# Optimization experiments

Measured on AMD Instinct MI355X. Metric: run time of the kernel, lower is better.

The kernel has to match this reference:

```python
import jax, jax.numpy as jnp
import numpy as np

TOP_K = 2

def setup_inputs() -> dict:
    key = jax.random.key(0)
    ks = jax.random.split(key, 8)
    B, S, D = 2, 2048, 1024
    N_r, N_s = 16, 2
    u = jax.random.normal(ks[0], (B, S, D), dtype=jnp.float32)
    centroids = jax.random.normal(ks[1], (N_r, D), dtype=jnp.float32)
    expert_biases = jnp.zeros((N_r,), dtype=jnp.float32)
    # routed expert Linear params: y = u @ W.T + b, W stored [E, d_out, d_in]
    Wr = jax.random.normal(ks[2], (N_r, D, D), dtype=jnp.float32) * (1.0 / np.sqrt(D))
    br = jax.random.normal(ks[3], (N_r, D), dtype=jnp.float32) * 0.01
    Ws = jax.random.normal(ks[4], (N_s, D, D), dtype=jnp.float32) * (1.0 / np.sqrt(D))
    bs = jax.random.normal(ks[5], (N_s, D), dtype=jnp.float32) * 0.01
    return {"u": u, "centroids": centroids, "expert_biases": expert_biases,
            "Wr": Wr, "br": br, "Ws": Ws, "bs": bs}

def reference(u, centroids, expert_biases, Wr, br, Ws, bs):
    N_r = centroids.shape[0]
    N_s = Ws.shape[0]
    # routing scores over experts
    raw_scores = jnp.einsum('bsd,ed->bse', u, centroids)          # [B,S,E]
    s = jax.nn.softmax(raw_scores + expert_biases, axis=-1)
    # scatter top-k softmax values (un-renormalized, as in the source) into gates
    topk_vals, topk_idx = jax.lax.top_k(s, TOP_K)                  # [B,S,K]
    g_topk = jnp.sum(jax.nn.one_hot(topk_idx, N_r, dtype=s.dtype) * topk_vals[..., None], axis=-2)  # [B,S,E]
    # dense per-expert Linear for all tokens, then gated combine (faithful to source)
    xe = jnp.einsum('bsd,eod->bseo', u, Wr) + br                   # [B,S,E,D]
    routed = jnp.einsum('bse,bseo->bso', g_topk, xe)               # [B,S,D]
    # shared experts: mean of N_s dense Linears
    shared = (jnp.einsum('bsd,eod->bso', u, Ws) + jnp.sum(bs, axis=0)) / N_s
    return u + routed + shared
```

## Files before the change

kernel.cpp:

```cpp
#include <hip/hip_runtime.h>

typedef unsigned short u16x8 __attribute__((ext_vector_type(8)));
typedef short          s16x8 __attribute__((ext_vector_type(8)));
typedef float          f32x4 __attribute__((ext_vector_type(4)));

#define NTOK   4096
#define DMODEL 1024
#define NEXP   16
#define TOPK   2
#define BK     32
#define NK     (DMODEL / BK)
#define MAXT   128

__device__ inline unsigned short f2bf(float f) {
    unsigned int x = __float_as_uint(f);
    x += 0x7fffu + ((x >> 16) & 1u);
    return (unsigned short)(x >> 16);
}
__device__ inline float bf2f(unsigned short h) {
    unsigned int x = ((unsigned int)h) << 16;
    return __uint_as_float(x);
}

__device__ inline void gld16(const void* g, void* l) {
    __builtin_amdgcn_global_load_lds(
        (const __attribute__((address_space(1))) void*)g,
        (__attribute__((address_space(3))) void*)l, 16, 0, 0);
}

#define NWR8  (NEXP * DMODEL * DMODEL / 8)
#define NWS8  (DMODEL * DMODEL / 8)
#define NB8   ((NEXP + 1) * DMODEL / 8)
#define RBLK  (NTOK / 4)
#define CBLK  ((NWR8 + NWS8 + NB8 + 255) / 256)

__global__ void prep_kernel(const float* __restrict__ u,
                            const float* __restrict__ cent,
                            const float* __restrict__ ebias,
                            const float* __restrict__ Wr,
                            const float* __restrict__ br,
                            const float* __restrict__ Ws,
                            const float* __restrict__ bs,
                            unsigned short* __restrict__ ub,
                            unsigned short* __restrict__ w17,
                            float* __restrict__ b17,
                            float* __restrict__ topk_g,
                            int*   __restrict__ topk_i) {
    int bid = blockIdx.x;
    if (bid >= RBLK) {
        int id = (bid - RBLK) * 256 + threadIdx.x;
        if (id < NWR8) {
            size_t base = (size_t)id * 8;
            f32x4 a = *(const f32x4*)&Wr[base];
            f32x4 b = *(const f32x4*)&Wr[base + 4];
            u16x8 o;
#pragma unroll
            for (int i = 0; i < 4; i++) { o[i] = f2bf(a[i]); o[i + 4] = f2bf(b[i]); }
            *(u16x8*)&w17[base] = o;
        } else if (id < NWR8 + NWS8) {
            size_t base = (size_t)(id - NWR8) * 8;
            f32x4 a0 = *(const f32x4*)&Ws[base];
            f32x4 b0 = *(const f32x4*)&Ws[base + 4];
            f32x4 a1 = *(const f32x4*)&Ws[(size_t)DMODEL * DMODEL + base];
            f32x4 b1 = *(const f32x4*)&Ws[(size_t)DMODEL * DMODEL + base + 4];
            u16x8 o;
#pragma unroll
            for (int i = 0; i < 4; i++) {
                o[i]     = f2bf(a0[i] + a1[i]);
                o[i + 4] = f2bf(b0[i] + b1[i]);
            }
            *(u16x8*)&w17[(size_t)NEXP * DMODEL * DMODEL + base] = o;
        } else if (id < NWR8 + NWS8 + NB8) {
            int base = (id - NWR8 - NWS8) * 8;
#pragma unroll
            for (int i = 0; i < 8; i++) {
                int idx = base + i;
                b17[idx] = idx < NEXP * DMODEL
                    ? br[idx]
                    : bs[idx - NEXP * DMODEL] + bs[idx - NEXP * DMODEL + DMODEL];
            }
        }
        return;
    }
    int wid  = threadIdx.x >> 6;
    int lane = threadIdx.x & 63;
    int t = bid * 4 + wid;
    const float* urow = u + (size_t)t * DMODEL;

    double acc[NEXP];
#pragma unroll
    for (int e = 0; e < NEXP; e++) acc[e] = 0.0;

    for (int j = 0; j < DMODEL / 64; j++) {
        int d = j * 64 + lane;
        float uf = urow[d];
        ub[(size_t)t * DMODEL + d] = f2bf(uf);
        double uv = (double)uf;
#pragma unroll
        for (int e = 0; e < NEXP; e++)
            acc[e] += uv * (double)cent[e * DMODEL + d];
    }
#pragma unroll
    for (int e = 0; e < NEXP; e++) {
        for (int off = 32; off; off >>= 1)
            acc[e] += __shfl_xor(acc[e], off);
    }
    if (lane == 0) {
        double mx = -1e300;
#pragma unroll
        for (int e = 0; e < NEXP; e++) {
            acc[e] += (double)ebias[e];
            if (acc[e] > mx) mx = acc[e];
        }
        double ex[NEXP], den = 0.0;
#pragma unroll
        for (int e = 0; e < NEXP; e++) { ex[e] = exp(acc[e] - mx); den += ex[e]; }
        int i1 = -1, i2 = -1;
        double v1 = -1.0, v2 = -1.0;
        for (int e = 0; e < NEXP; e++) {
            double v = ex[e];
            if (v > v1)      { v2 = v1; i2 = i1; v1 = v; i1 = e; }
            else if (v > v2) { v2 = v;  i2 = e; }
        }
        topk_g[t * 2 + 0] = (float)(v1 / den);
        topk_g[t * 2 + 1] = (float)(v2 / den);
        topk_i[t * 2 + 0] = i1;
        topk_i[t * 2 + 1] = i2;
    }
}

__global__ void build_all(const float* __restrict__ topk_g,
                          const int*   __restrict__ topk_i,
                          int* __restrict__ cnt,
                          int* __restrict__ tokL,
                          float* __restrict__ gateL,
                          int* __restrict__ idL,
                          int* __restrict__ desc,
                          int* __restrict__ numT) {
    __shared__ int scnt[NEXP];
    int tid = threadIdx.x;
    if (tid < NEXP) scnt[tid] = 0;
    __syncthreads();
    for (int id = tid; id < NTOK * TOPK; id += 1024) {
        int e = topk_i[id];
        int pos = atomicAdd(&scnt[e], 1);
        tokL[e * NTOK + pos]  = id >> 1;
        gateL[e * NTOK + pos] = topk_g[id];
        idL[e * NTOK + pos]   = id;
    }
    __syncthreads();
    if (tid == 0) {
        int s = 0;
        for (int mt = 0; mt < NTOK / 128; mt++) desc[s++] = (NEXP << 16) | mt;
        for (int e = 0; e < NEXP; e++) {
            cnt[e] = scnt[e];
            int nt = (scnt[e] + 127) >> 7;
            for (int m = 0; m < nt; m++) desc[s++] = (e << 16) | m;
        }
        numT[0] = s;
    }
}

__global__ __launch_bounds__(256, 4)
void moe_gemm(const unsigned short* __restrict__ ub,
              const unsigned short* __restrict__ w17,
              const float* __restrict__ b17,
              const int*   __restrict__ cnt,
              const int*   __restrict__ tokL,
              const float* __restrict__ gateL,
              const int*   __restrict__ idL,
              const int*   __restrict__ desc,
              const int*   __restrict__ numT,
              const float* __restrict__ u,
              float* __restrict__ out,
              unsigned short* __restrict__ y) {
    int bid = blockIdx.x;
    int tile = bid >> 3;
    int n0 = (bid & 7) * 128;
    if (tile >= numT[0]) return;
    int d = desc[tile];
    int e = d >> 16;
    int row0 = (d & 0xffff) << 7;
    bool is_shared = (e == NEXP);
    int count = is_shared ? NTOK : cnt[e];

    __shared__ __align__(16) unsigned short As[2][128 * BK];
    __shared__ __align__(16) unsigned short Bs[2][128 * BK];

    int t = threadIdx.x;
    int lane = t & 63, wid = t >> 6;
    int wm = wid >> 1, wn = wid & 1;
    int lr = lane & 15, lk4 = lane >> 4;
    int rchunk = (lk4 ^ ((lr >> 1) & 3)) * 8;

    int srow = lane >> 2;
    int scs  = ((lane & 3) ^ ((lane >> 3) & 3)) * 8;

    const int* tl = tokL + e * NTOK;
    const unsigned short* asrc[2];
    const unsigned short* bsrc[2];
    const unsigned short* bb = w17 + (size_t)e * DMODEL * DMODEL + (size_t)n0 * DMODEL;
#pragma unroll
    for (int p = 0; p < 2; p++) {
        int gi = row0 + wid * 32 + p * 16 + srow;
        int tok = is_shared ? gi : tl[gi < count ? gi : count - 1];
        asrc[p] = ub + (size_t)tok * DMODEL + scs;
        bsrc[p] = bb + (size_t)(wid * 32 + p * 16 + srow) * DMODEL + scs;
    }

#define STAGE(buf, kt) do {                                                     \
    int _k0 = (kt) * BK;                                                        \
    _Pragma("unroll")                                                           \
    for (int p = 0; p < 2; p++) {                                               \
        int r = wid * 32 + p * 16;                                              \
        gld16(asrc[p] + _k0, &As[buf][r * BK]);                                 \
        gld16(bsrc[p] + _k0, &Bs[buf][r * BK]);                                 \
    } } while (0)

    f32x4 acc[4][4];
#pragma unroll
    for (int i = 0; i < 4; i++)
#pragma unroll
        for (int j = 0; j < 4; j++)
#pragma unroll
            for (int v = 0; v < 4; v++) acc[i][j][v] = 0.0f;

    STAGE(0, 0);
    int cur = 0;
    for (int kt = 0; kt < NK; kt++) {
        if (kt + 1 < NK) {
            STAGE(cur ^ 1, kt + 1);
            asm volatile("s_waitcnt vmcnt(4)" ::: "memory");
        } else {
            asm volatile("s_waitcnt vmcnt(0)" ::: "memory");
        }
        __builtin_amdgcn_s_barrier();

        __builtin_amdgcn_s_setprio(1);
        s16x8 b[4];
#pragma unroll
        for (int j = 0; j < 4; j++)
            b[j] = *(const s16x8*)&Bs[cur][(wn * 64 + j * 16 + lr) * BK + rchunk];
#pragma unroll
        for (int i = 0; i < 4; i++) {
            s16x8 a = *(const s16x8*)&As[cur][(wm * 64 + i * 16 + lr) * BK + rchunk];
#pragma unroll
            for (int j = 0; j < 4; j++)
                acc[i][j] = __builtin_amdgcn_mfma_f32_16x16x32_bf16(a, b[j], acc[i][j], 0, 0, 0);
        }
        __builtin_amdgcn_s_setprio(0);

        asm volatile("" ::: "memory");
        __builtin_amdgcn_s_barrier();
        cur ^= 1;
    }
#undef STAGE

    const float* be = b17 + e * DMODEL;
    if (is_shared) {
#pragma unroll
        for (int i = 0; i < 4; i++) {
#pragma unroll
            for (int v = 0; v < 4; v++) {
                int row = row0 + wm * 64 + i * 16 + lk4 * 4 + v;
#pragma unroll
                for (int j = 0; j < 4; j++) {
                    int col = n0 + wn * 64 + j * 16 + lr;
                    size_t idx = (size_t)row * DMODEL + col;
                    out[idx] = u[idx] + 0.5f * (acc[i][j][v] + be[col]);
                }
            }
        }
    } else {
#pragma unroll
        for (int i = 0; i < 4; i++) {
#pragma unroll
            for (int v = 0; v < 4; v++) {
                int gi = row0 + wm * 64 + i * 16 + lk4 * 4 + v;
                if (gi < count) {
                    int id = idL[e * NTOK + gi];
                    float g = gateL[e * NTOK + gi];
                    unsigned short* yr = y + (size_t)id * DMODEL;
#pragma unroll
                    for (int j = 0; j < 4; j++) {
                        int col = n0 + wn * 64 + j * 16 + lr;
                        yr[col] = f2bf(g * (acc[i][j][v] + be[col]));
                    }
                }
            }
        }
    }
}

__global__ void combine_kernel(const unsigned short* __restrict__ y,
                               float* __restrict__ out) {
    int idx = blockIdx.x * 256 + threadIdx.x;
    int tk = idx >> 7;
    int d8 = (idx & 127) * 8;
    size_t base = (size_t)tk * DMODEL + d8;
    u16x8 a = *(const u16x8*)&y[(size_t)(tk * 2) * DMODEL + d8];
    u16x8 b = *(const u16x8*)&y[(size_t)(tk * 2 + 1) * DMODEL + d8];
    f32x4 o0 = *(const f32x4*)&out[base];
    f32x4 o1 = *(const f32x4*)&out[base + 4];
#pragma unroll
    for (int v = 0; v < 4; v++) {
        o0[v] += bf2f(a[v]) + bf2f(b[v]);
        o1[v] += bf2f(a[v + 4]) + bf2f(b[v + 4]);
    }
    *(f32x4*)&out[base] = o0;
    *(f32x4*)&out[base + 4] = o1;
}

extern "C" void kernel_launch(void* const* d_in, const int* in_sizes, int n_in,
                              void* d_out, int out_size, void* d_ws, size_t ws_size,
                              hipStream_t stream) {
    const float* u    = (const float*)d_in[0];
    const float* cent = (const float*)d_in[1];
    const float* eb   = (const float*)d_in[2];
    const float* Wr   = (const float*)d_in[3];
    const float* br   = (const float*)d_in[4];
    const float* Ws   = (const float*)d_in[5];
    const float* bs   = (const float*)d_in[6];
    float* out = (float*)d_out;

    char* ws = (char*)d_ws;
    size_t off = 0;
    auto take = [&](size_t b) { size_t o = off; off += (b + 255) & ~(size_t)255; return o; };
    float* topk_g = (float*)(ws + take(NTOK * TOPK * 4));
    int*   topk_i = (int*)  (ws + take(NTOK * TOPK * 4));
    int*   cnt    = (int*)  (ws + take(64 * 4));
    int*   tokL   = (int*)  (ws + take((size_t)NEXP * NTOK * 4));
    float* gateL  = (float*)(ws + take((size_t)NEXP * NTOK * 4));
    int*   idL    = (int*)  (ws + take((size_t)NEXP * NTOK * 4));
    int*   desc   = (int*)  (ws + take(MAXT * 4));
    int*   numT   = (int*)  (ws + take(64));
    float* b17    = (float*)(ws + take((size_t)(NEXP + 1) * DMODEL * 4));
    unsigned short* ub  = (unsigned short*)(ws + take((size_t)NTOK * DMODEL * 2));
    unsigned short* w17 = (unsigned short*)(ws + take((size_t)(NEXP + 1) * DMODEL * DMODEL * 2));
    unsigned short* y   = (unsigned short*)(ws + take((size_t)NTOK * TOPK * DMODEL * 2));

    prep_kernel<<<RBLK + CBLK, 256, 0, stream>>>(
        u, cent, eb, Wr, br, Ws, bs, ub, w17, b17, topk_g, topk_i);
    build_all<<<1, 1024, 0, stream>>>(topk_g, topk_i, cnt, tokL, gateL, idL, desc, numT);
    moe_gemm<<<8 * MAXT, 256, 0, stream>>>(
        ub, w17, b17, cnt, tokL, gateL, idL, desc, numT, u, out, y);
    combine_kernel<<<(NTOK * DMODEL / 8) / 256, 256, 0, stream>>>(y, out);
}
```

Before: 100.0 us.

## Enlarge MoE GEMM tiles to 256x256x64 and parallelize expert bucketing

```diff
diff --git a/kernel.cpp b/kernel.cpp
--- a/kernel.cpp
+++ b/kernel.cpp
@@ -8,9 +8,9 @@
 #define DMODEL 1024
 #define NEXP   16
 #define TOPK   2
-#define BK     32
-#define NK     (DMODEL / BK)
-#define MAXT   128
+#define BKG    64
+#define NKT    (DMODEL / BKG)
+#define MAXT2  64
 
 __device__ inline unsigned short f2bf(float f) {
     unsigned int x = __float_as_uint(f);
@@ -129,39 +129,37 @@
     }
 }
 
-__global__ void build_all(const float* __restrict__ topk_g,
-                          const int*   __restrict__ topk_i,
-                          int* __restrict__ cnt,
-                          int* __restrict__ tokL,
-                          float* __restrict__ gateL,
-                          int* __restrict__ idL,
-                          int* __restrict__ desc,
-                          int* __restrict__ numT) {
-    __shared__ int scnt[NEXP];
-    int tid = threadIdx.x;
-    if (tid < NEXP) scnt[tid] = 0;
+__global__ void bucket16(const float* __restrict__ tg,
+                         const int*   __restrict__ ti,
+                         int* __restrict__ cnt,
+                         int* __restrict__ tokL,
+                         float* __restrict__ gateL,
+                         int* __restrict__ idL) {
+    int e = blockIdx.x;
+    __shared__ int base;
+    if (threadIdx.x == 0) base = 0;
     __syncthreads();
-    for (int id = tid; id < NTOK * TOPK; id += 1024) {
-        int e = topk_i[id];
-        int pos = atomicAdd(&scnt[e], 1);
-        tokL[e * NTOK + pos]  = id >> 1;
-        gateL[e * NTOK + pos] = topk_g[id];
-        idL[e * NTOK + pos]   = id;
+    int lane = threadIdx.x & 63;
+    for (int c0 = 0; c0 < NTOK * TOPK; c0 += 256) {
+        int id = c0 + threadIdx.x;
+        bool m = (ti[id] == e);
+        unsigned long long mask = __ballot(m);
+        int wcnt = __popcll(mask);
+        int wpos = 0;
+        if (lane == 0) wpos = atomicAdd(&base, wcnt);
+        wpos = __shfl(wpos, 0);
+        if (m) {
+            int pos = wpos + __popcll(mask & ((1ull << lane) - 1ull));
+            tokL[e * NTOK + pos]  = id >> 1;
+            gateL[e * NTOK + pos] = tg[id];
+            idL[e * NTOK + pos]   = id;
+        }
     }
     __syncthreads();
-    if (tid == 0) {
-        int s = 0;
-        for (int mt = 0; mt < NTOK / 128; mt++) desc[s++] = (NEXP << 16) | mt;
-        for (int e = 0; e < NEXP; e++) {
-            cnt[e] = scnt[e];
-            int nt = (scnt[e] + 127) >> 7;
-            for (int m = 0; m < nt; m++) desc[s++] = (e << 16) | m;
-        }
-        numT[0] = s;
-    }
-}
-
-__global__ __launch_bounds__(256, 4)
+    if (threadIdx.x == 0) cnt[e] = base;
+}
+
+__global__ __launch_bounds__(512, 2)
 void moe_gemm(const unsigned short* __restrict__ ub,
               const unsigned short* __restrict__ w17,
               const float* __restrict__ b17,
@@ -169,57 +167,63 @@
               const int*   __restrict__ tokL,
               const float* __restrict__ gateL,
               const int*   __restrict__ idL,
-              const int*   __restrict__ desc,
-              const int*   __restrict__ numT,
               const float* __restrict__ u,
               float* __restrict__ out,
               unsigned short* __restrict__ y) {
     int bid = blockIdx.x;
-    int tile = bid >> 3;
-    int n0 = (bid & 7) * 128;
-    if (tile >= numT[0]) return;
-    int d = desc[tile];
-    int e = d >> 16;
-    int row0 = (d & 0xffff) << 7;
+    int np   = bid & 3;
+    int tile = bid >> 2;
+    int e, row0;
+    if (tile < NTOK / 256) {
+        e = NEXP; row0 = tile << 8;
+    } else {
+        int rt = tile - NTOK / 256;
+        int ee = 0;
+        for (; ee < NEXP; ee++) {
+            int nt = (cnt[ee] + 255) >> 8;
+            if (rt < nt) break;
+            rt -= nt;
+        }
+        if (ee >= NEXP) return;
+        e = ee; row0 = rt << 8;
+    }
     bool is_shared = (e == NEXP);
     int count = is_shared ? NTOK : cnt[e];
-
-    __shared__ __align__(16) unsigned short As[2][128 * BK];
-    __shared__ __align__(16) unsigned short Bs[2][128 * BK];
+    int n0 = np * 256;
+
+    __shared__ __align__(16) unsigned short As[2][256 * BKG];
+    __shared__ __align__(16) unsigned short Bs[2][256 * BKG];
 
     int t = threadIdx.x;
     int lane = t & 63, wid = t >> 6;
-    int wm = wid >> 1, wn = wid & 1;
+    int wm = wid >> 2, wn = wid & 3;
     int lr = lane & 15, lk4 = lane >> 4;
-    int rchunk = (lk4 ^ ((lr >> 1) & 3)) * 8;
-
-    int srow = lane >> 2;
-    int scs  = ((lane & 3) ^ ((lane >> 3) & 3)) * 8;
+
+    int srow8 = lane >> 3;
+    int scs   = ((lane & 7) ^ srow8) * 8;
 
     const int* tl = tokL + e * NTOK;
-    const unsigned short* asrc[2];
-    const unsigned short* bsrc[2];
+    int tokA[4];
+#pragma unroll
+    for (int r = 0; r < 4; r++) {
+        int gi = row0 + r * 64 + wid * 8 + srow8;
+        tokA[r] = is_shared ? gi : tl[gi < count ? gi : count - 1];
+    }
     const unsigned short* bb = w17 + (size_t)e * DMODEL * DMODEL + (size_t)n0 * DMODEL;
-#pragma unroll
-    for (int p = 0; p < 2; p++) {
-        int gi = row0 + wid * 32 + p * 16 + srow;
-        int tok = is_shared ? gi : tl[gi < count ? gi : count - 1];
-        asrc[p] = ub + (size_t)tok * DMODEL + scs;
-        bsrc[p] = bb + (size_t)(wid * 32 + p * 16 + srow) * DMODEL + scs;
-    }
-
-#define STAGE(buf, kt) do {                                                     \
-    int _k0 = (kt) * BK;                                                        \
-    _Pragma("unroll")                                                           \
-    for (int p = 0; p < 2; p++) {                                               \
-        int r = wid * 32 + p * 16;                                              \
-        gld16(asrc[p] + _k0, &As[buf][r * BK]);                                 \
-        gld16(bsrc[p] + _k0, &Bs[buf][r * BK]);                                 \
+
+#define STAGE(buf, kt) do {                                                        \
+    int _k0 = (kt) * BKG;                                                          \
+    _Pragma("unroll")                                                              \
+    for (int r = 0; r < 4; r++) {                                                  \
+        gld16(&ub[(size_t)tokA[r] * DMODEL + _k0 + scs],                           \
+              &As[buf][(r * 64 + wid * 8) * BKG]);                                 \
+        gld16(&bb[(size_t)(r * 64 + wid * 8 + srow8) * DMODEL + _k0 + scs],        \
+              &Bs[buf][(r * 64 + wid * 8) * BKG]);                                 \
     } } while (0)
 
-    f32x4 acc[4][4];
-#pragma unroll
-    for (int i = 0; i < 4; i++)
+    f32x4 acc[8][4];
+#pragma unroll
+    for (int i = 0; i < 8; i++)
 #pragma unroll
         for (int j = 0; j < 4; j++)
 #pragma unroll
@@ -227,26 +231,31 @@
 
     STAGE(0, 0);
     int cur = 0;
-    for (int kt = 0; kt < NK; kt++) {
-        if (kt + 1 < NK) {
+    for (int kt = 0; kt < NKT; kt++) {
+        if (kt + 1 < NKT) {
             STAGE(cur ^ 1, kt + 1);
-            asm volatile("s_waitcnt vmcnt(4)" ::: "memory");
+            asm volatile("s_waitcnt vmcnt(8)" ::: "memory");
         } else {
             asm volatile("s_waitcnt vmcnt(0)" ::: "memory");
         }
         __builtin_amdgcn_s_barrier();
 
         __builtin_amdgcn_s_setprio(1);
-        s16x8 b[4];
-#pragma unroll
-        for (int j = 0; j < 4; j++)
-            b[j] = *(const s16x8*)&Bs[cur][(wn * 64 + j * 16 + lr) * BK + rchunk];
-#pragma unroll
-        for (int i = 0; i < 4; i++) {
-            s16x8 a = *(const s16x8*)&As[cur][(wm * 64 + i * 16 + lr) * BK + rchunk];
+#pragma unroll
+        for (int ks = 0; ks < 2; ks++) {
+            s16x8 b[4];
 #pragma unroll
             for (int j = 0; j < 4; j++)
-                acc[i][j] = __builtin_amdgcn_mfma_f32_16x16x32_bf16(a, b[j], acc[i][j], 0, 0, 0);
+                b[j] = *(const s16x8*)&Bs[cur][(wn * 64 + j * 16 + lr) * BKG
+                                               + (((ks * 4 + lk4) ^ (lr & 7)) * 8)];
+#pragma unroll
+            for (int i = 0; i < 8; i++) {
+                s16x8 a = *(const s16x8*)&As[cur][(wm * 128 + i * 16 + lr) * BKG
+                                                  + (((ks * 4 + lk4) ^ (lr & 7)) * 8)];
+#pragma unroll
+                for (int j = 0; j < 4; j++)
+                    acc[i][j] = __builtin_amdgcn_mfma_f32_16x16x32_bf16(a, b[j], acc[i][j], 0, 0, 0);
+            }
         }
         __builtin_amdgcn_s_setprio(0);
 
@@ -259,10 +268,10 @@
     const float* be = b17 + e * DMODEL;
     if (is_shared) {
 #pragma unroll
-        for (int i = 0; i < 4; i++) {
+        for (int i = 0; i < 8; i++) {
 #pragma unroll
             for (int v = 0; v < 4; v++) {
-                int row = row0 + wm * 64 + i * 16 + lk4 * 4 + v;
+                int row = row0 + wm * 128 + i * 16 + lk4 * 4 + v;
 #pragma unroll
                 for (int j = 0; j < 4; j++) {
                     int col = n0 + wn * 64 + j * 16 + lr;
@@ -273,10 +282,10 @@
         }
     } else {
 #pragma unroll
-        for (int i = 0; i < 4; i++) {
+        for (int i = 0; i < 8; i++) {
 #pragma unroll
             for (int v = 0; v < 4; v++) {
-                int gi = row0 + wm * 64 + i * 16 + lk4 * 4 + v;
+                int gi = row0 + wm * 128 + i * 16 + lk4 * 4 + v;
                 if (gi < count) {
                     int id = idL[e * NTOK + gi];
                     float g = gateL[e * NTOK + gi];
@@ -332,8 +341,6 @@
     int*   tokL   = (int*)  (ws + take((size_t)NEXP * NTOK * 4));
     float* gateL  = (float*)(ws + take((size_t)NEXP * NTOK * 4));
     int*   idL    = (int*)  (ws + take((size_t)NEXP * NTOK * 4));
-    int*   desc   = (int*)  (ws + take(MAXT * 4));
-    int*   numT   = (int*)  (ws + take(64));
     float* b17    = (float*)(ws + take((size_t)(NEXP + 1) * DMODEL * 4));
     unsigned short* ub  = (unsigned short*)(ws + take((size_t)NTOK * DMODEL * 2));
     unsigned short* w17 = (unsigned short*)(ws + take((size_t)(NEXP + 1) * DMODEL * DMODEL * 2));
@@ -341,8 +348,8 @@
 
     prep_kernel<<<RBLK + CBLK, 256, 0, stream>>>(
         u, cent, eb, Wr, br, Ws, bs, ub, w17, b17, topk_g, topk_i);
-    build_all<<<1, 1024, 0, stream>>>(topk_g, topk_i, cnt, tokL, gateL, idL, desc, numT);
-    moe_gemm<<<8 * MAXT, 256, 0, stream>>>(
-        ub, w17, b17, cnt, tokL, gateL, idL, desc, numT, u, out, y);
+    bucket16<<<NEXP, 256, 0, stream>>>(topk_g, topk_i, cnt, tokL, gateL, idL);
+    moe_gemm<<<4 * MAXT2, 512, 0, stream>>>(
+        ub, w17, b17, cnt, tokL, gateL, idL, u, out, y);
     combine_kernel<<<(NTOK * DMODEL / 8) / 256, 256, 0, stream>>>(y, out);
 }
```

Result: no change. 101.1 us (+1.1%).
